# Kernel optimization log

Measured on AMD Instinct MI355X. Metric: run time of the kernel, lower is better.

Reference implementation:

```python
import jax, jax.numpy as jnp
import numpy as np
from math import factorial, pi

# ---- static module config (ModelEncodeDecodeSimple defaults) ----
B_IN, B_OUT = 30, 10        # input / output bandwidths
F_IN, F_OUT = 2, 5          # feature channels
BATCH = 512
N_ALPHA, MAX_BETA, N_BETA = 6, pi / 160.0, 1  # s2_near_identity_grid args


def _wigner_d(l, beta):
    """Wigner-d matrix d^l_{m',m}(beta), rows m'=-l..l, cols m=-l..l (quantum norm, CS phase)."""
    cb, sb = np.cos(beta / 2.0), np.sin(beta / 2.0)
    d = np.zeros((2 * l + 1, 2 * l + 1))
    for i, mp in enumerate(range(-l, l + 1)):
        for j, m in enumerate(range(-l, l + 1)):
            pref = np.sqrt(float(factorial(l + m) * factorial(l - m) * factorial(l + mp) * factorial(l - mp)))
            tot = 0.0
            for s in range(max(0, m - mp), min(l + m, l - mp) + 1):
                den = factorial(l + m - s) * factorial(s) * factorial(mp - m + s) * factorial(l - mp - s)
                tot += ((-1.0) ** (mp - m + s) / den) * cb ** (2 * l + m - mp - 2 * s) * sb ** (mp - m + 2 * s)
            d[i, j] = pref * tot
    return d


def _quad_weights(b):
    """Driscoll-Healy quadrature weights on the SOFT beta grid (lie_learn S2.quadrature_weights)."""
    k = np.arange(b)
    betas = pi * (2 * np.arange(2 * b) + 1) / (4 * b)
    return (2.0 / b) * np.sin(betas) * np.array(
        [np.sum(np.sin((2 * j + 1) * (2 * k + 1) * pi / (4 * b)) / (2 * k + 1)) for j in range(2 * b)])


# ---- precomputed constants (all static, numpy) ----
_betas_in = pi * (2 * np.arange(2 * B_IN) + 1) / (4 * B_IN)
_w = _quad_weights(B_IN)
NSPEC_S2 = B_OUT ** 2  # sum over l<b_out of (2l+1)
W_S2 = np.zeros((2 * B_IN, NSPEC_S2), dtype=np.float32)   # w_k * d^l_{m0}(beta_k)
FREQ_IN = np.zeros(NSPEC_S2, dtype=np.int64)              # alpha FFT bin for each (l,m)
for l in range(B_OUT):
    d_m0 = np.stack([_wigner_d(l, bb)[:, l] for bb in _betas_in])  # [2b_in, 2l+1]
    W_S2[:, l * l:l * l + 2 * l + 1] = (_w[:, None] * d_m0).astype(np.float32)
    FREQ_IN[l * l:l * l + 2 * l + 1] = np.arange(-l, l + 1) % (2 * B_IN)

# kernel grid: s2_near_identity_grid(n_alpha=6, max_beta=pi/160, n_beta=1)
_gb = np.arange(1, N_BETA + 1) * MAX_BETA / N_BETA
_ga = np.linspace(0, 2 * pi, N_ALPHA, endpoint=False)
GB, GA = np.meshgrid(_gb, _ga, indexing='ij')
GB, GA = GB.ravel(), GA.ravel()
N_GRID = GB.size
K_FT = np.zeros((NSPEC_S2, N_GRID), dtype=np.complex64)   # D^l_{m0}(alpha_g, beta_g, 0)
for l in range(B_OUT):
    for g in range(N_GRID):
        d_m0 = _wigner_d(l, GB[g])[:, l]
        K_FT[l * l:l * l + 2 * l + 1, g] = d_m0 * np.exp(-1j * np.arange(-l, l + 1) * GA[g])
SCALING = np.float32(1.0 / np.sqrt(N_GRID * F_IN * (B_OUT ** 4.0) / (B_IN ** 2.0)))

# SO(3) inverse-FFT Wigner blocks at output betas, scaled by (2l+1) (s2cnn so3_ifft convention)
_betas_out = pi * (2 * np.arange(2 * B_OUT) + 1) / (4 * B_OUT)
D_SO3 = [np.stack([_wigner_d(l, bb) for bb in _betas_out]).astype(np.float32) * (2 * l + 1)
         for l in range(B_OUT)]


def s2conv(x, kernel, bias):
    Bsz = x.shape[0]
    # --- S2 FFT of input: FFT over alpha, then quadrature-weighted Wigner contraction over beta ---
    Xf = jnp.fft.fft(x, axis=-1)                     # [B, f_in, 2b_in(beta), 2b_in(alpha-freq)] c64
    gx = Xf[:, :, :, FREQ_IN]                        # [B, f_in, 2b_in, nspec]
    fhat = jnp.einsum('bfks,ks->sbf', gx, W_S2.astype(np.complex64))   # [nspec, B, f_in]
    # --- kernel spherical FT on the near-identity grid ---
    yhat = jnp.einsum('iog,sg->sio', kernel * SCALING, K_FT)           # [nspec, f_in, f_out]
    # --- per-degree outer product (s2_mm, conj on kernel) + SO(3) spectral accumulation ---
    T = jnp.zeros((Bsz, F_OUT, 2 * B_OUT, 2 * B_OUT, 2 * B_OUT), dtype=fhat.dtype)
    for l in range(B_OUT):
        L = 2 * l + 1
        xl = fhat[l * l:l * l + L]                   # [L, B, f_in]
        yl = yhat[l * l:l * l + L]                   # [L, f_in, f_out]
        zl = jnp.einsum('mbi,nio->mnbo', xl, jnp.conj(yl))             # z^l_{mn}
        contrib = jnp.einsum('mnbo,kmn->bokmn', zl, D_SO3[l].astype(np.complex64))
        mi = np.arange(-l, l + 1) % (2 * B_OUT)
        T = T.at[:, :, :, mi[:, None], mi[None, :]].add(contrib)
    # --- inverse FFT over (alpha, gamma); SOFT convention multiplies by (2b)^2; take real part ---
    out = jnp.fft.ifft2(T, axes=(-2, -1)).real * float((2 * B_OUT) ** 2)
    return out + bias                                # [B, f_out, 2b_out, 2b_out, 2b_out]


def setup_inputs() -> dict:
    key = jax.random.key(0)
    k1, k2, k3 = jax.random.split(key, 3)
    x1 = jax.random.normal(k1, (BATCH, F_IN, 2 * B_IN, 2 * B_IN), dtype=jnp.float32)
    kernel = jax.random.normal(k2, (F_IN, F_OUT, N_GRID), dtype=jnp.float32)
    bias = jax.random.normal(k3, (1, F_OUT, 1, 1, 1), dtype=jnp.float32)
    return {"x1": x1, "kernel": kernel, "bias": bias}


def reference(x1, kernel, bias):
    return s2conv(x1, kernel, bias)
```

## Files before the change

### kernel.cpp

```cpp
#include <hip/hip_runtime.h>
#include <math.h>
#include <stdint.h>


typedef _Float16 half8 __attribute__((ext_vector_type(8)));
typedef float    f32x4 __attribute__((ext_vector_type(4)));

#define WS_W    128
#define WS_Y    17760
#define WS_EM   19776
#define WS_RT   20992
#define WS_PACK 21184
#define WS_AP   21952
#define WS_FH   107968
#define WS_DT   220608
#define WS_F    234908

#define IX_Y0    3300
#define IX_EM0   4300
#define IX_RT0   4900
#define IX_PACK0 5090
#define IX_AP0   5805
#define IX_DT0   177837
#define N_SETUP  192137

__device__ __forceinline__ double ipow_d(double x, int e) {
    double r = 1.0;
    for (int i = 0; i < e; ++i) r *= x;
    return r;
}

__device__ double dsmall(int l, int mp, int m, double beta) {
    double fact[20];
    fact[0] = 1.0;
    for (int i = 1; i < 20; ++i) fact[i] = fact[i - 1] * (double)i;
    double cb = cos(0.5 * beta), sb = sin(0.5 * beta);
    double pref = sqrt(fact[l + m] * fact[l - m] * fact[l + mp] * fact[l - mp]);
    int s0 = m - mp; if (s0 < 0) s0 = 0;
    int s1 = l + m;  if (l - mp < s1) s1 = l - mp;
    double tot = 0.0;
    for (int s = s0; s <= s1; ++s) {
        double den = fact[l + m - s] * fact[s] * fact[mp - m + s] * fact[l - mp - s];
        double sgn = ((mp - m + s) & 1) ? -1.0 : 1.0;
        tot += sgn / den * ipow_d(cb, 2 * l + m - mp - 2 * s) * ipow_d(sb, mp - m + 2 * s);
    }
    return pref * tot;
}

extern "C" __global__ void k_setup_w(float* wsf) {
    double* w = (double*)wsf;
    int t = threadIdx.x;
    if (t < 60) {
        double beta = M_PI * (2 * t + 1) / 120.0;
        double sum = 0.0;
        for (int k = 0; k < 30; ++k)
            sum += sin((double)((2 * t + 1) * (2 * k + 1)) * M_PI / 120.0) / (double)(2 * k + 1);
        w[t] = (2.0 / 30.0) * sin(beta) * sum;
    }
}

extern "C" __global__ void k_setup_const(float* wsf, const float* __restrict__ kern) {
    const double* w = (const double*)wsf;
    const int tri[11] = {0, 1, 3, 6, 10, 15, 21, 28, 36, 45, 55};
    int idx = blockIdx.x * 64 + threadIdx.x;
    if (idx < IX_Y0) {
        int k = idx / 55, smi = idx % 55;
        int l = 0; while (smi >= tri[l + 1]) ++l;
        int m = smi - tri[l];
        double beta = M_PI * (2 * k + 1) / 120.0;
        wsf[WS_W + idx] = (float)(w[k] * dsmall(l, m, 0, beta));
    } else if (idx < IX_EM0) {
        int i3 = idx - IX_Y0;
        int o = i3 / 200, r5 = i3 % 200;
        int s = r5 / 2, i = r5 % 2;
        int l = 0; while ((l + 1) * (l + 1) <= s) ++l;
        int n = s - l * l - l;
        double dv = dsmall(l, n, 0, M_PI / 160.0);
        const double SC = 1.0 / sqrt(6.0 * 2.0 * 10000.0 / 900.0);
        double ar = 0.0, ai = 0.0;
        for (int g = 0; g < 6; ++g) {
            double kv = (double)kern[i * 30 + o * 6 + g];
            double ang = (double)n * M_PI * (double)g / 3.0;
            ar += kv * cos(ang);
            ai -= kv * sin(ang);
        }
        ((float2*)(wsf + WS_Y))[i3] = make_float2((float)(SC * dv * ar), (float)(SC * dv * ai));
    } else if (idx < IX_RT0) {
        int t = idx - IX_EM0; int m = t / 60, j = t % 60;
        double a = 2.0 * M_PI * (double)(m * j) / 60.0;
        ((float2*)(wsf + WS_EM))[t] = make_float2((float)cos(a), (float)(-sin(a)));
    } else if (idx < IX_PACK0) {
        int r = idx - IX_RT0;
        int m = r / 19, nn = r % 19, n = nn - 9;
        int a = n < 0 ? -n : n;
        int lmin = m > a ? m : a;
        int tL = lmin * (lmin - 1);
        int base = tL * (2 * lmin - 1) / 3 + ((3 * tL) >> 1) + lmin;
        int p0 = base + m * (2 * lmin + 1) + n + lmin;
        ((int*)(wsf + WS_RT))[r] = p0 | (lmin << 10) | (m << 14);
    } else if (idx < IX_AP0) {
        int p = idx - IX_PACK0;
        int l = 0, bcur = 0;
        for (;;) { int bs = (l + 1) * (2 * l + 1); if (p < bcur + bs) break; bcur += bs; ++l; }
        int r = p - bcur; int L = 2 * l + 1;
        int m = r / L; int n = r % L - l;
        int smi = tri[l] + m; int sf = l * l + l + n;
        ((int*)(wsf + WS_PACK))[p] = smi * 128 + sf;
    } else if (idx < IX_DT0) {
        int ap = idx - IX_AP0;
        int j = ap & 7, lane = (ap >> 3) & 63, tc = ap >> 9;
        int t = tc % 28, c = tc / 28;
        int pq = t * 16 + (lane & 15);
        int kidx = c * 32 + ((lane >> 4) << 3) + j;
        double val = 0.0;
        if (pq < 400 && kidx < 380) {
            int r = kidx >> 1, cpart = kidx & 1;
            int m = r / 19, nn = r % 19, n = nn - 9;
            int p = pq / 20, q = pq % 20;
            int th = ((m * p + n * q) % 20 + 20) % 20;
            double wm = m ? 2.0 : 1.0;
            double ang = M_PI * (double)th / 10.0;
            val = cpart ? (-wm * sin(ang)) : (wm * cos(ang));
        }
        ((_Float16*)(wsf + WS_AP))[ap] = (_Float16)val;
    } else if (idx < N_SETUP) {
        int i6 = idx - IX_DT0;
        int p = i6 / 20, k = i6 % 20;
        int l = 0, bcur = 0;
        for (;;) { int bs = (l + 1) * (2 * l + 1); if (p < bcur + bs) break; bcur += bs; ++l; }
        int r = p - bcur; int L = 2 * l + 1;
        int m = r / L; int n = r % L - l;
        double beta = M_PI * (2 * k + 1) / 40.0;
        wsf[WS_DT + i6] = (float)((double)L * dsmall(l, m, n, beta));
    }
}

extern "C" __global__ void __launch_bounds__(256) k_fhat(const float* __restrict__ x,
                                                          float* __restrict__ wsf) {
    __shared__ float  xs[3600];
    __shared__ float2 ems[610];
    __shared__ float2 Y[600];
    int tid = threadIdx.x;
    int bi = blockIdx.x;
    const float4* xp = (const float4*)(x + bi * 3600);
    for (int t = tid; t < 900; t += 256) ((float4*)xs)[t] = xp[t];
    const float2* gEm = (const float2*)(wsf + WS_EM);
    for (int t = tid; t < 600; t += 256) {
        int m = t / 60, j = t - m * 60;
        ems[m * 61 + j] = gEm[t];
    }
    __syncthreads();
    for (int it = tid; it < 600; it += 256) {
        int k = it / 10, m = it - k * 10;
        const float*  row = xs + k * 60;
        const float2* em  = ems + m * 61;
        float ar = 0.f, ai = 0.f;
        #pragma unroll 12
        for (int j = 0; j < 60; ++j) {
            float xv = row[j];
            float2 e = em[j];
            ar += xv * e.x; ai += xv * e.y;
        }
        Y[it] = make_float2(ar, ai);
    }
    __syncthreads();
    if (tid < 55) {
        int smi = tid;
        const int tri[11] = {0, 1, 3, 6, 10, 15, 21, 28, 36, 45, 55};
        int l = 0; while (smi >= tri[l + 1]) ++l;
        int m = smi - tri[l];
        const float* gW = wsf + WS_W;
        float ar = 0.f, ai = 0.f;
        for (int kk = 0; kk < 60; ++kk) {
            float wv = gW[kk * 55 + smi];
            float2 y = Y[kk * 10 + m];
            ar += wv * y.x; ai += wv * y.y;
        }
        int b = bi >> 1, i = bi & 1;
        ((float2*)(wsf + WS_FH))[b * 110 + smi * 2 + i] = make_float2(ar, ai);
    }
}

extern "C" __global__ void __launch_bounds__(256) k_zF(float* __restrict__ wsf) {
    __shared__ float2 zsh[2860];
    __shared__ float4 fbl4[110];
    __shared__ float4 yol4[500];
    int tid = threadIdx.x;
    int n0 = blockIdx.x * 64;
    int PO0 = n0 / 20;
    int bf = PO0 / 5;

    const float4* gfh4 = (const float4*)(wsf + WS_FH);
    for (int t = tid; t < 110; t += 256) {
        int bsel = t / 55, i55 = t - bsel * 55;
        int b = bf + bsel;
        fbl4[t] = (b < 512) ? gfh4[b * 55 + i55] : make_float4(0.f, 0.f, 0.f, 0.f);
    }
    for (int t = tid; t < 500; t += 256) yol4[t] = ((const float4*)(wsf + WS_Y))[t];
    __syncthreads();
    const int* gPack = (const int*)(wsf + WS_PACK);
    for (int pp = 0; pp < 4; ++pp) {
        int po = PO0 + pp;
        int b_loc = po / 5 - bf, o = po % 5;
        for (int p = tid; p < 715; p += 256) {
            int pk = gPack[p];
            int smi = pk >> 7, sf = pk & 127;
            float4 f = fbl4[b_loc * 55 + smi];
            float4 y = yol4[o * 100 + sf];
            float zr = f.x * y.x + f.y * y.y + f.z * y.z + f.w * y.w;
            float zi = f.y * y.x - f.x * y.y + f.w * y.z - f.z * y.w;
            zsh[pp * 715 + p] = make_float2(zr, zi);
        }
    }
    __syncthreads();

    int col = tid & 63;
    int ko  = (n0 + col) % 20;
    int pp  = ((n0 % 20) + col) / 20;
    int gg  = (n0 >> 4) + (col >> 4);
    int c15 = col & 15;
    const float* gDT = wsf + WS_DT;
    uint32_t*    gF  = (uint32_t*)(wsf + WS_F);
    const int baseL[10] = {0, 1, 7, 22, 50, 95, 161, 252, 372, 525};
    const float2* zp = zsh + pp * 715;
    for (int it = tid; it < 12160; it += 256) {
        int r = it >> 6;
        int m = r / 19;
        int n = r - m * 19 - 9;
        int a = n < 0 ? -n : n;
        int lmin = m > a ? m : a;
        float fr = 0.f, fi = 0.f;
        #pragma unroll
        for (int l = 0; l < 10; ++l) {
            int p = baseL[l] + m * (2 * l + 1) + n + l;
            int pc = p < 0 ? 0 : p;
            float d = gDT[pc * 20 + ko];
            float2 z = zp[pc];
            d = (l >= lmin) ? d : 0.f;
            fr += d * z.x;
            fi += d * z.y;
        }
        int chunk = r >> 4, w5 = (2 * r) & 31;
        int qp = w5 >> 3, dwi = (w5 & 7) >> 1;
        union { _Float16 h[2]; uint32_t u; } fv;
        fv.h[0] = (_Float16)fr; fv.h[1] = (_Float16)fi;
        gF[((chunk * 3200 + gg) * 64 + (qp * 16 + c15)) * 4 + dwi] = fv.u;
    }
    if (tid < 128) {
        int cc = tid >> 1, dwi = 2 + (tid & 1);
        int g2 = (n0 >> 4) + (cc >> 4);
        gF[((11 * 3200 + g2) * 64 + (48 + (cc & 15))) * 4 + dwi] = 0u;
    }
}

extern "C" __global__ void __launch_bounds__(256) k_gemm2(const float* __restrict__ wsf,
                                                           const float* __restrict__ bias,
                                                           float* __restrict__ out) {
    int tid = threadIdx.x;
    int n0 = blockIdx.x * 64;
    int wave = tid >> 6, lane = tid & 63;
    int g0 = n0 >> 4;
    const half8* gA = (const half8*)(wsf + WS_AP);
    const half8* gB = (const half8*)(wsf + WS_F);
    int t0 = wave * 7;
    int ntile = (wave < 3) ? 7 : 4;

    f32x4 acc[7][4];
    #pragma unroll
    for (int tt = 0; tt < 7; ++tt)
        #pragma unroll
        for (int f = 0; f < 4; ++f) acc[tt][f] = (f32x4){0.f, 0.f, 0.f, 0.f};

    half8 bufB[2][4], bufA[2][7];
    #pragma unroll
    for (int f = 0; f < 4; ++f) bufB[0][f] = gB[(g0 + f) * 64 + lane];
    #pragma unroll
    for (int tt = 0; tt < 7; ++tt)
        if (tt < ntile) bufA[0][tt] = gA[(t0 + tt) * 64 + lane];

    #pragma unroll
    for (int c = 0; c < 12; ++c) {
        const int cur = c & 1, nxt = cur ^ 1;
        if (c < 11) {
            #pragma unroll
            for (int f = 0; f < 4; ++f)
                bufB[nxt][f] = gB[((c + 1) * 3200 + g0 + f) * 64 + lane];
            #pragma unroll
            for (int tt = 0; tt < 7; ++tt)
                if (tt < ntile) bufA[nxt][tt] = gA[((c + 1) * 28 + t0 + tt) * 64 + lane];
        }
        #pragma unroll
        for (int tt = 0; tt < 7; ++tt) {
            if (tt < ntile) {
                #pragma unroll
                for (int f = 0; f < 4; ++f)
                    acc[tt][f] = __builtin_amdgcn_mfma_f32_16x16x32_f16(bufA[cur][tt], bufB[cur][f], acc[tt][f], 0, 0, 0);
            }
        }
    }

    int quad4 = (lane >> 4) << 2, col15 = lane & 15;
    float bo_f[4];
    #pragma unroll
    for (int f = 0; f < 4; ++f) bo_f[f] = bias[((n0 + f * 16 + col15) / 20) % 5];
    #pragma unroll
    for (int tt = 0; tt < 7; ++tt) {
        if (tt < ntile) {
            int pqb = (t0 + tt) * 16 + quad4;
            #pragma unroll
            for (int f = 0; f < 4; ++f) {
                int n = n0 + f * 16 + col15;
                float bo = bo_f[f];
                float4 v = make_float4(acc[tt][f].x + bo, acc[tt][f].y + bo,
                                       acc[tt][f].z + bo, acc[tt][f].w + bo);
                *(float4*)(out + n * 400 + pqb) = v;
            }
        }
    }
}

extern "C" void kernel_launch(void* const* d_in, const int* in_sizes, int n_in,
                              void* d_out, int out_size, void* d_ws, size_t ws_size,
                              hipStream_t stream) {
    const float* x    = (const float*)d_in[0];
    const float* kern = (const float*)d_in[1];
    const float* bias = (const float*)d_in[2];
    float* out = (float*)d_out;
    float* wsf = (float*)d_ws;
    k_setup_w    <<<1,    64,  0, stream>>>(wsf);
    k_setup_const<<<3003, 64,  0, stream>>>(wsf, kern);
    k_fhat       <<<1024, 256, 0, stream>>>(x, wsf);
    k_zF         <<<800,  256, 0, stream>>>(wsf);
    k_gemm2      <<<800,  256, 0, stream>>>(wsf, bias, out);
}
```

Baseline: 198.6 us.

## Skip zero Wigner terms in k_zF via lmin specialization and split rows across blocks

```diff
diff --git a/kernel.cpp b/kernel.cpp
--- a/kernel.cpp
+++ b/kernel.cpp
@@ -106,7 +106,7 @@
         int m = r / L; int n = r % L - l;
         int smi = tri[l] + m; int sf = l * l + l + n;
         ((int*)(wsf + WS_PACK))[p] = smi * 128 + sf;
-    } else if (idx < IX_DT0) {
+    } else if (idx < IX_AP0 + 172032 && idx >= IX_AP0) {
         int ap = idx - IX_AP0;
         int j = ap & 7, lane = (ap >> 3) & 63, tc = ap >> 9;
         int t = tc % 28, c = tc / 28;
@@ -181,12 +181,33 @@
     }
 }
 
+template<int L>
+__device__ __forceinline__ void fsum(int m, int n, int ko, const float* __restrict__ gDT,
+                                     const float2* __restrict__ zp, float& fr, float& fi) {
+    const int baseL[10] = {0, 1, 7, 22, 50, 95, 161, 252, 372, 525};
+    float dv[10 - L];
+    float2 zv[10 - L];
+    #pragma unroll
+    for (int l = L; l < 10; ++l) {
+        int p = baseL[l] + m * (2 * l + 1) + n + l;
+        dv[l - L] = gDT[p * 20 + ko];
+        zv[l - L] = zp[p];
+    }
+    #pragma unroll
+    for (int l = L; l < 10; ++l) {
+        fr += dv[l - L] * zv[l - L].x;
+        fi += dv[l - L] * zv[l - L].y;
+    }
+}
+
 extern "C" __global__ void __launch_bounds__(256) k_zF(float* __restrict__ wsf) {
     __shared__ float2 zsh[2860];
     __shared__ float4 fbl4[110];
     __shared__ float4 yol4[500];
     int tid = threadIdx.x;
-    int n0 = blockIdx.x * 64;
+    int half = blockIdx.x & 1;
+    int nb   = blockIdx.x >> 1;
+    int n0 = nb * 64;
     int PO0 = n0 / 20;
     int bf = PO0 / 5;
 
@@ -221,24 +242,25 @@
     int c15 = col & 15;
     const float* gDT = wsf + WS_DT;
     uint32_t*    gF  = (uint32_t*)(wsf + WS_F);
-    const int baseL[10] = {0, 1, 7, 22, 50, 95, 161, 252, 372, 525};
     const float2* zp = zsh + pp * 715;
-    for (int it = tid; it < 12160; it += 256) {
-        int r = it >> 6;
+    for (int it = tid; it < 6080; it += 256) {
+        int r = __builtin_amdgcn_readfirstlane(((it >> 6) << 1) | half);
         int m = r / 19;
         int n = r - m * 19 - 9;
         int a = n < 0 ? -n : n;
         int lmin = m > a ? m : a;
         float fr = 0.f, fi = 0.f;
-        #pragma unroll
-        for (int l = 0; l < 10; ++l) {
-            int p = baseL[l] + m * (2 * l + 1) + n + l;
-            int pc = p < 0 ? 0 : p;
-            float d = gDT[pc * 20 + ko];
-            float2 z = zp[pc];
-            d = (l >= lmin) ? d : 0.f;
-            fr += d * z.x;
-            fi += d * z.y;
+        switch (lmin) {
+            case 0: fsum<0>(m, n, ko, gDT, zp, fr, fi); break;
+            case 1: fsum<1>(m, n, ko, gDT, zp, fr, fi); break;
+            case 2: fsum<2>(m, n, ko, gDT, zp, fr, fi); break;
+            case 3: fsum<3>(m, n, ko, gDT, zp, fr, fi); break;
+            case 4: fsum<4>(m, n, ko, gDT, zp, fr, fi); break;
+            case 5: fsum<5>(m, n, ko, gDT, zp, fr, fi); break;
+            case 6: fsum<6>(m, n, ko, gDT, zp, fr, fi); break;
+            case 7: fsum<7>(m, n, ko, gDT, zp, fr, fi); break;
+            case 8: fsum<8>(m, n, ko, gDT, zp, fr, fi); break;
+            default: fsum<9>(m, n, ko, gDT, zp, fr, fi); break;
         }
         int chunk = r >> 4, w5 = (2 * r) & 31;
         int qp = w5 >> 3, dwi = (w5 & 7) >> 1;
@@ -246,7 +268,7 @@
         fv.h[0] = (_Float16)fr; fv.h[1] = (_Float16)fi;
         gF[((chunk * 3200 + gg) * 64 + (qp * 16 + c15)) * 4 + dwi] = fv.u;
     }
-    if (tid < 128) {
+    if (half == 0 && tid < 128) {
         int cc = tid >> 1, dwi = 2 + (tid & 1);
         int g2 = (n0 >> 4) + (cc >> 4);
         gF[((11 * 3200 + g2) * 64 + (48 + (cc & 15))) * 4 + dwi] = 0u;
@@ -330,6 +352,6 @@
     k_setup_w    <<<1,    64,  0, stream>>>(wsf);
     k_setup_const<<<3003, 64,  0, stream>>>(wsf, kern);
     k_fhat       <<<1024, 256, 0, stream>>>(x, wsf);
-    k_zF         <<<800,  256, 0, stream>>>(wsf);
+    k_zF         <<<1600, 256, 0, stream>>>(wsf);
     k_gemm2      <<<800,  256, 0, stream>>>(wsf, bias, out);
 }
```

Measured after the change: 186.2 us. 6.3% less time.
